# Kernel tuning notes

Hardware: AMD Instinct MI355X
Metric: run time of the kernel (lower is better)

The kernel has to match this reference:

```python
import jax, jax.numpy as jnp
import numpy as np

EPS = 1e-5

def _layernorm(x, gamma, beta):
    mu = jnp.mean(x, axis=-1, keepdims=True)
    var = jnp.mean(jnp.square(x - mu), axis=-1, keepdims=True)
    return (x - mu) * jax.lax.rsqrt(var + EPS) * gamma + beta

def setup_inputs() -> dict:
    key = jax.random.key(0)
    ks = jax.random.split(key, 8)
    B, T, H = 8, 4096, 512
    s = 1.0 / np.sqrt(H)  # torch LSTM init scale
    return {
        "x": jax.random.normal(ks[0], (B, T, H), jnp.float32),
        "W_ih": jax.random.uniform(ks[1], (4 * H, H), jnp.float32, -s, s),
        "W_hh": jax.random.uniform(ks[2], (4 * H, H), jnp.float32, -s, s),
        "b_ih": jax.random.uniform(ks[3], (4 * H,), jnp.float32, -s, s),
        "b_hh": jax.random.uniform(ks[4], (4 * H,), jnp.float32, -s, s),
        "gamma": jnp.ones((H,), jnp.float32),
        "beta": jnp.zeros((H,), jnp.float32),
        "W_lin": jax.random.uniform(ks[5], (H, H), jnp.float32, -s, s),
        "b_lin": jax.random.uniform(ks[6], (H,), jnp.float32, -s, s),
    }

def _lstm(res, W_ih, W_hh, b_ih, b_hh):
    # res: [B, T, H]; torch gate order: i, f, g, o
    B, T, H = res.shape
    # precompute input contributions for all timesteps: [T, B, 4H]
    x_proj = jnp.einsum('bth,gh->tbg', res, W_ih) + (b_ih + b_hh)

    def step(carry, xp):
        h, c = carry  # [B, H] each
        gates = xp + h @ W_hh.T  # [B, 4H]
        i, f, g, o = jnp.split(gates, 4, axis=-1)
        i = jax.nn.sigmoid(i)
        f = jax.nn.sigmoid(f)
        g = jnp.tanh(g)
        o = jax.nn.sigmoid(o)
        c = f * c + i * g
        h = o * jnp.tanh(c)
        return (h, c), h

    h0 = jnp.zeros((B, H), res.dtype)
    c0 = jnp.zeros((B, H), res.dtype)
    (hT, cT), hs = jax.lax.scan(step, (h0, c0), x_proj)
    out = jnp.transpose(hs, (1, 0, 2))  # [B, T, H]
    return out, (hT[None], cT[None])

def reference(x, W_ih, W_hh, b_ih, b_hh, gamma, beta, W_lin, b_lin):
    res = _layernorm(x, gamma, beta)
    out, out_state = _lstm(res, W_ih, W_hh, b_ih, b_hh)
    gate = jax.nn.silu(res @ W_lin.T + b_lin)
    out = out * gate + res
    return (out, out_state)
```

## Files before the change

### kernel.cpp

```cpp
#include <hip/hip_runtime.h>
#include <math.h>

#define NB 8
#define HID 512

typedef unsigned int uint4v __attribute__((ext_vector_type(4)));

__device__ __forceinline__ float sigf(float x) { return 1.0f / (1.0f + __expf(-x)); }
__device__ __forceinline__ float tanhf_(float x) {
    return 2.0f / (1.0f + __expf(-2.0f * x)) - 1.0f;
}

__global__ void init_ws_kernel(unsigned long long* h_bufs) {
    h_bufs[blockIdx.x * 256 + threadIdx.x] = 0ull;
}

__global__ void ln_kernel(const float* __restrict__ x, const float* __restrict__ gamma,
                          const float* __restrict__ beta, float* __restrict__ res,
                          int t0, int chsh) {
    int wid = threadIdx.x >> 6, lane = threadIdx.x & 63;
    int rl = blockIdx.x * 4 + wid;
    int b = rl >> chsh, i = rl & ((1 << chsh) - 1);
    const float* xr = x + (long long)(b * 4096 + t0 + i) * HID;
    float4 u0 = *(const float4*)(xr + lane * 4);
    float4 u1 = *(const float4*)(xr + 256 + lane * 4);
    float s = u0.x + u0.y + u0.z + u0.w + u1.x + u1.y + u1.z + u1.w;
#pragma unroll
    for (int m = 1; m < 64; m <<= 1) s += __shfl_xor(s, m, 64);
    float mu = s * (1.0f / 512.0f);
    float d[8] = {u0.x - mu, u0.y - mu, u0.z - mu, u0.w - mu,
                  u1.x - mu, u1.y - mu, u1.z - mu, u1.w - mu};
    float q = d[0]*d[0] + d[1]*d[1] + d[2]*d[2] + d[3]*d[3] +
              d[4]*d[4] + d[5]*d[5] + d[6]*d[6] + d[7]*d[7];
#pragma unroll
    for (int m = 1; m < 64; m <<= 1) q += __shfl_xor(q, m, 64);
    float rs = rsqrtf(q * (1.0f / 512.0f) + 1e-5f);
    float4 g0 = *(const float4*)(gamma + lane * 4);
    float4 g1 = *(const float4*)(gamma + 256 + lane * 4);
    float4 b0 = *(const float4*)(beta + lane * 4);
    float4 b1 = *(const float4*)(beta + 256 + lane * 4);
    float* rr = res + (long long)rl * HID;
    float4 o0, o1;
    o0.x = d[0] * rs * g0.x + b0.x; o0.y = d[1] * rs * g0.y + b0.y;
    o0.z = d[2] * rs * g0.z + b0.z; o0.w = d[3] * rs * g0.w + b0.w;
    o1.x = d[4] * rs * g1.x + b1.x; o1.y = d[5] * rs * g1.y + b1.y;
    o1.z = d[6] * rs * g1.z + b1.z; o1.w = d[7] * rs * g1.w + b1.w;
    *(float4*)(rr + lane * 4) = o0;
    *(float4*)(rr + 256 + lane * 4) = o1;
}

template <int MODE>
__launch_bounds__(256, 2)
__global__ void gemm_nt(const float* __restrict__ A, const float* __restrict__ B,
                        const float* __restrict__ bias1, const float* __restrict__ bias2,
                        float* __restrict__ C, int N) {
    __shared__ float As[16][132];
    __shared__ float Bs[16][132];
    int tid = threadIdx.x;
    int tx = tid & 15, ty = tid >> 4;
    int r0 = blockIdx.x * 128;
    int j0 = blockIdx.y * 128;
    int arow = tid >> 2, ac = (tid & 3) * 4;

    float acc[8][8] = {};

    for (int kt = 0; kt < 512; kt += 16) {
        float4 a0 = *(const float4*)(A + (long long)(r0 + arow) * 512 + kt + ac);
        float4 a1 = *(const float4*)(A + (long long)(r0 + arow + 64) * 512 + kt + ac);
        float4 b0 = *(const float4*)(B + (long long)(j0 + arow) * 512 + kt + ac);
        float4 b1 = *(const float4*)(B + (long long)(j0 + arow + 64) * 512 + kt + ac);
        __syncthreads();
        As[ac + 0][arow] = a0.x; As[ac + 1][arow] = a0.y;
        As[ac + 2][arow] = a0.z; As[ac + 3][arow] = a0.w;
        As[ac + 0][arow + 64] = a1.x; As[ac + 1][arow + 64] = a1.y;
        As[ac + 2][arow + 64] = a1.z; As[ac + 3][arow + 64] = a1.w;
        Bs[ac + 0][arow] = b0.x; Bs[ac + 1][arow] = b0.y;
        Bs[ac + 2][arow] = b0.z; Bs[ac + 3][arow] = b0.w;
        Bs[ac + 0][arow + 64] = b1.x; Bs[ac + 1][arow + 64] = b1.y;
        Bs[ac + 2][arow + 64] = b1.z; Bs[ac + 3][arow + 64] = b1.w;
        __syncthreads();
#pragma unroll
        for (int kk = 0; kk < 16; kk++) {
            float a[8], bb[8];
            *(float4*)(a)      = *(const float4*)&As[kk][ty * 8];
            *(float4*)(a + 4)  = *(const float4*)&As[kk][ty * 8 + 4];
            *(float4*)(bb)     = *(const float4*)&Bs[kk][tx * 8];
            *(float4*)(bb + 4) = *(const float4*)&Bs[kk][tx * 8 + 4];
#pragma unroll
            for (int i = 0; i < 8; i++)
#pragma unroll
                for (int j = 0; j < 8; j++) acc[i][j] += a[i] * bb[j];
        }
    }

    float bv[8];
#pragma unroll
    for (int jj = 0; jj < 8; jj++) {
        int j = j0 + tx * 8 + jj;
        bv[jj] = (MODE == 0) ? (bias1[j] + bias2[j]) : bias1[j];
    }
#pragma unroll
    for (int ii = 0; ii < 8; ii++) {
        long long r = r0 + ty * 8 + ii;
        float* crow = C + r * (long long)N + j0 + tx * 8;
        float v[8];
#pragma unroll
        for (int jj = 0; jj < 8; jj++) {
            float tv = acc[ii][jj] + bv[jj];
            if (MODE == 1) tv = tv * sigf(tv);
            v[jj] = tv;
        }
        float4 o0, o1;
        o0.x = v[0]; o0.y = v[1]; o0.z = v[2]; o0.w = v[3];
        o1.x = v[4]; o1.y = v[5]; o1.z = v[6]; o1.w = v[7];
        *(float4*)(crow) = o0;
        *(float4*)(crow + 4) = o1;
    }
}

__launch_bounds__(256, 1)
__global__ void scan_kernel(const float* __restrict__ W_hh,
                            const float* __restrict__ xp,
                            const float* __restrict__ resv,
                            const float* __restrict__ gatev,
                            float* __restrict__ out,
                            unsigned long long* __restrict__ h_fast,
                            unsigned long long* __restrict__ h_safe,
                            float* __restrict__ c_buf,
                            int t0, int chsh) {
    const int CH = 1 << chsh;
    int b = blockIdx.x & 7, w = blockIdx.x >> 3;
    int tid = threadIdx.x;
    int kg = tid & 15, rq = tid >> 4;
    int slot = w * 16 + rq;

    __shared__ __align__(16) float h_s[2][512];

    float wreg[4][32];
#pragma unroll
    for (int g = 0; g < 4; g++) {
        const float* wr = W_hh + (long long)((g << 9) + slot) * 512 + (kg << 5);
#pragma unroll
        for (int q = 0; q < 8; q++) {
            float4 u = *(const float4*)(wr + q * 4);
            wreg[g][q * 4 + 0] = u.x; wreg[g][q * 4 + 1] = u.y;
            wreg[g][q * 4 + 2] = u.z; wreg[g][q * 4 + 3] = u.w;
        }
    }

    float c_reg = 0.0f;
    if (t0 > 0 && kg == 0) c_reg = c_buf[(b << 9) + slot];

    int mode = 0;

    const int pr0 = 2 * tid;
    const int n_w  = tid >> 1;
    const int pg_w = (n_w & ~7) | ((n_w ^ (n_w >> 3)) & 7);
    const int fi_w = (pg_w << 2) | (pr0 & 3);

    for (int i = 0; i < CH; i++) {
        int t = t0 + i;
        int rl = (b << chsh) + i;

        float xpv0 = 0, xpv1 = 0, xpv2 = 0, xpv3 = 0, gv = 0, rv = 0;
        if (kg == 0) {
            const float* xr = xp + (long long)rl * 2048 + slot;
            xpv0 = xr[0]; xpv1 = xr[512]; xpv2 = xr[1024]; xpv3 = xr[1536];
            gv = gatev[rl * 512 + slot];
            rv = resv[rl * 512 + slot];
        }

        float acc0 = 0, acc1 = 0, acc2 = 0, acc3 = 0;
        if (t > 0) {
            const int par = (t - 1) & 1;
            const unsigned exp_tag = (unsigned)t;
            float h0 = 0.0f, h1 = 0.0f;
            bool got = false;

            if (mode == 0) {
                const unsigned long long* fb = h_fast + par * 4096 + (b << 9);
                uint4v p4;
                int tries = 0;
                while (true) {
                    asm volatile(
                        "global_load_dwordx4 %0, %1, off nt\n\t"
                        "s_waitcnt vmcnt(0)"
                        : "=v"(p4) : "v"(fb + pr0) : "memory");
                    if (p4[1] == exp_tag && p4[3] == exp_tag) {
                        h0 = __uint_as_float(p4[0]);
                        h1 = __uint_as_float(p4[2]);
                        got = true;
                        break;
                    }
                    if (++tries > 768) { mode = 1; break; }
                }
            }
            if (!got) {
                const unsigned long long* sb = h_safe + par * 4096 + (b << 9);
                unsigned long long v0 = 0, v1 = 0;
                if (mode == 1) {
                    bool g0 = false, g1 = false;
                    int tr = 0;
                    while (true) {
                        if (!g0) {
                            v0 = __hip_atomic_load(sb + pr0, __ATOMIC_RELAXED,
                                                   __HIP_MEMORY_SCOPE_AGENT);
                            g0 = ((unsigned)(v0 >> 32) == exp_tag);
                        }
                        if (!g1) {
                            v1 = __hip_atomic_load(sb + pr0 + 1, __ATOMIC_RELAXED,
                                                   __HIP_MEMORY_SCOPE_AGENT);
                            g1 = ((unsigned)(v1 >> 32) == exp_tag);
                        }
                        if (g0 && g1) break;
                        if (++tr > (1 << 15)) { mode = 2; break; }
                    }
                } else {
                    v0 = __hip_atomic_load(sb + pr0, __ATOMIC_RELAXED,
                                           __HIP_MEMORY_SCOPE_AGENT);
                    v1 = __hip_atomic_load(sb + pr0 + 1, __ATOMIC_RELAXED,
                                           __HIP_MEMORY_SCOPE_AGENT);
                }
                h0 = __uint_as_float((unsigned)v0);
                h1 = __uint_as_float((unsigned)v1);
            }

            int p = t & 1;
            *(float2*)&h_s[p][fi_w] = make_float2(h0, h1);
            __syncthreads();
            float hv[32];
#pragma unroll
            for (int q = 0; q < 8; q++) {
                int pg = (kg << 3) + (q ^ (kg & 7));
                float4 u = *(const float4*)&h_s[p][pg << 2];
                hv[q * 4 + 0] = u.x; hv[q * 4 + 1] = u.y;
                hv[q * 4 + 2] = u.z; hv[q * 4 + 3] = u.w;
            }
#pragma unroll
            for (int j = 0; j < 32; j++) {
                acc0 += hv[j] * wreg[0][j];
                acc1 += hv[j] * wreg[1][j];
                acc2 += hv[j] * wreg[2][j];
                acc3 += hv[j] * wreg[3][j];
            }
            acc0 += __shfl_xor(acc0, 1, 64); acc0 += __shfl_xor(acc0, 2, 64);
            acc0 += __shfl_xor(acc0, 4, 64); acc0 += __shfl_xor(acc0, 8, 64);
            acc1 += __shfl_xor(acc1, 1, 64); acc1 += __shfl_xor(acc1, 2, 64);
            acc1 += __shfl_xor(acc1, 4, 64); acc1 += __shfl_xor(acc1, 8, 64);
            acc2 += __shfl_xor(acc2, 1, 64); acc2 += __shfl_xor(acc2, 2, 64);
            acc2 += __shfl_xor(acc2, 4, 64); acc2 += __shfl_xor(acc2, 8, 64);
            acc3 += __shfl_xor(acc3, 1, 64); acc3 += __shfl_xor(acc3, 2, 64);
            acc3 += __shfl_xor(acc3, 4, 64); acc3 += __shfl_xor(acc3, 8, 64);
        }

        if (kg == 0) {
            float iv = sigf(acc0 + xpv0);
            float fv = sigf(acc1 + xpv1);
            float gt = tanhf_(acc2 + xpv2);
            float ov = sigf(acc3 + xpv3);
            c_reg = fv * c_reg + iv * gt;
            float h = ov * tanhf_(c_reg);
            unsigned long long pkt =
                ((unsigned long long)(unsigned)(t + 1) << 32) |
                (unsigned long long)__float_as_uint(h);
            __hip_atomic_store(h_safe + (t & 1) * 4096 + (b << 9) + slot, pkt,
                               __ATOMIC_RELAXED, __HIP_MEMORY_SCOPE_AGENT);
            unsigned long long* fp = h_fast + (t & 1) * 4096 + (b << 9) + slot;
            asm volatile("global_store_dwordx2 %0, %1, off sc0"
                         :: "v"(fp), "v"(pkt) : "memory");
            out[(long long)((b << 12) + t) * 512 + slot] = h * gv + rv;
            if (t == 4095) {
                out[16777216 + (b << 9) + slot] = h;
                out[16777216 + 4096 + (b << 9) + slot] = c_reg;
            }
            if (i == CH - 1) c_buf[(b << 9) + slot] = c_reg;
        }
    }
}

extern "C" void kernel_launch(void* const* d_in, const int* in_sizes, int n_in,
                              void* d_out, int out_size, void* d_ws, size_t ws_size,
                              hipStream_t stream) {
    const float* x     = (const float*)d_in[0];
    const float* W_ih  = (const float*)d_in[1];
    const float* W_hh  = (const float*)d_in[2];
    const float* b_ih  = (const float*)d_in[3];
    const float* b_hh  = (const float*)d_in[4];
    const float* gamma = (const float*)d_in[5];
    const float* beta  = (const float*)d_in[6];
    const float* W_lin = (const float*)d_in[7];
    const float* b_lin = (const float*)d_in[8];
    float* out = (float*)d_out;

    const size_t small_bytes = 16384ull * 8 + 4096ull * 4;
    int CH = 256;
    for (int cand = 4096; cand >= 256; cand >>= 1) {
        if ((size_t)98304 * cand + small_bytes <= ws_size) { CH = cand; break; }
    }
    int chsh = 31 - __builtin_clz(CH);

    float* ws      = (float*)d_ws;
    float* res_ch  = ws;
    float* gate_ch = res_ch + (size_t)8 * CH * 512;
    float* xp_ch   = gate_ch + (size_t)8 * CH * 512;
    unsigned long long* h_fast = (unsigned long long*)(xp_ch + (size_t)8 * CH * 2048);
    unsigned long long* h_safe = h_fast + 8192;
    float* c_buf   = (float*)(h_safe + 8192);

    init_ws_kernel<<<64, 256, 0, stream>>>(h_fast);

    int nchunks = 4096 / CH;
    for (int c = 0; c < nchunks; c++) {
        int t0 = c * CH;
        ln_kernel<<<8 * CH / 4, 256, 0, stream>>>(x, gamma, beta, res_ch, t0, chsh);
        gemm_nt<0><<<dim3(8 * CH / 128, 16), 256, 0, stream>>>(res_ch, W_ih, b_ih, b_hh,
                                                               xp_ch, 2048);
        gemm_nt<1><<<dim3(8 * CH / 128, 4), 256, 0, stream>>>(res_ch, W_lin, b_lin, b_lin,
                                                              gate_ch, 512);
        scan_kernel<<<256, 256, 0, stream>>>(W_hh, xp_ch, res_ch, gate_ch, out,
                                             h_fast, h_safe, c_buf, t0, chsh);
    }
}
```

Measured before the change: 7.330 ms.

## Prefetch xp/gate/res into double-buffered LDS and pipeline h polling loads

Result: faster. 6.702 ms (median of 2 runs) (-8.6%).

```diff
diff --git a/kernel.cpp b/kernel.cpp
--- a/kernel.cpp
+++ b/kernel.cpp
@@ -134,7 +134,11 @@
     int kg = tid & 15, rq = tid >> 4;
     int slot = w * 16 + rq;
 
-    __shared__ __align__(16) float h_s[2][512];
+    __shared__ __align__(16) float lds[13312];
+
+    const int ep_s = tid >> 2;
+    const int ep_g = tid & 3;
+    const int gr_s = tid & 63;
 
     float wreg[4][32];
 #pragma unroll
@@ -152,47 +156,69 @@
     if (t0 > 0 && kg == 0) c_reg = c_buf[(b << 9) + slot];
 
     int mode = 0;
-
     const int pr0 = 2 * tid;
     const int n_w  = tid >> 1;
     const int pg_w = (n_w & ~7) | ((n_w ^ (n_w >> 3)) & 7);
     const int fi_w = (pg_w << 2) | (pr0 & 3);
 
+    uint4v pa = {0, 0, 0, 0}, pb = {0, 0, 0, 0};
+    float4 pfx0 = {0,0,0,0}, pfx1 = {0,0,0,0}, pfx2 = {0,0,0,0}, pfx3 = {0,0,0,0};
+    float4 pfg0 = {0,0,0,0}, pfg1 = {0,0,0,0}, pfg2 = {0,0,0,0}, pfg3 = {0,0,0,0};
+
+    {
+        int row = (b << chsh) + ((ep_s < CH) ? ep_s : CH - 1);
+        const float* xr = xp + (long long)row * 2048 + (ep_g << 9) + (w << 4);
+        pfx0 = *(const float4*)(xr + 0);  pfx1 = *(const float4*)(xr + 4);
+        pfx2 = *(const float4*)(xr + 8);  pfx3 = *(const float4*)(xr + 12);
+        if (tid < 128) {
+            int row2 = (b << chsh) + gr_s;
+            const float* gr = (tid < 64 ? gatev : resv) + (long long)row2 * 512 + (w << 4);
+            pfg0 = *(const float4*)(gr + 0);  pfg1 = *(const float4*)(gr + 4);
+            pfg2 = *(const float4*)(gr + 8);  pfg3 = *(const float4*)(gr + 12);
+        }
+        asm volatile("s_waitcnt vmcnt(0)" ::: "memory");
+        float* xd = lds + 1024 + (ep_s << 6) + (ep_g << 4);
+        *(float4*)(xd + 0) = pfx0;  *(float4*)(xd + 4) = pfx1;
+        *(float4*)(xd + 8) = pfx2;  *(float4*)(xd + 12) = pfx3;
+        if (tid < 128) {
+            float* gd = lds + (tid < 64 ? 9216 : 11264) + (gr_s << 4);
+            *(float4*)(gd + 0) = pfg0;  *(float4*)(gd + 4) = pfg1;
+            *(float4*)(gd + 8) = pfg2;  *(float4*)(gd + 12) = pfg3;
+        }
+    }
+
     for (int i = 0; i < CH; i++) {
         int t = t0 + i;
-        int rl = (b << chsh) + i;
-
-        float xpv0 = 0, xpv1 = 0, xpv2 = 0, xpv3 = 0, gv = 0, rv = 0;
-        if (kg == 0) {
-            const float* xr = xp + (long long)rl * 2048 + slot;
-            xpv0 = xr[0]; xpv1 = xr[512]; xpv2 = xr[1024]; xpv3 = xr[1536];
-            gv = gatev[rl * 512 + slot];
-            rv = resv[rl * 512 + slot];
-        }
-
-        float acc0 = 0, acc1 = 0, acc2 = 0, acc3 = 0;
+        int es = i & 63;
+        int e = (i >> 6) & 1;
+        int p = t & 1;
+
+        float h0 = 0.0f, h1 = 0.0f;
         if (t > 0) {
             const int par = (t - 1) & 1;
             const unsigned exp_tag = (unsigned)t;
-            float h0 = 0.0f, h1 = 0.0f;
             bool got = false;
-
             if (mode == 0) {
-                const unsigned long long* fb = h_fast + par * 4096 + (b << 9);
-                uint4v p4;
+                const unsigned long long* fb = h_fast + par * 4096 + (b << 9) + pr0;
                 int tries = 0;
+                asm volatile("global_load_dwordx4 %0, %1, off nt"
+                             : "=v"(pa) : "v"(fb) : "memory");
                 while (true) {
-                    asm volatile(
-                        "global_load_dwordx4 %0, %1, off nt\n\t"
-                        "s_waitcnt vmcnt(0)"
-                        : "=v"(p4) : "v"(fb + pr0) : "memory");
-                    if (p4[1] == exp_tag && p4[3] == exp_tag) {
-                        h0 = __uint_as_float(p4[0]);
-                        h1 = __uint_as_float(p4[2]);
-                        got = true;
-                        break;
+                    asm volatile("global_load_dwordx4 %0, %1, off nt"
+                                 : "=v"(pb) : "v"(fb) : "memory");
+                    asm volatile("s_waitcnt vmcnt(1)" : "+v"(pa) :: "memory");
+                    if (pa[1] == exp_tag && pa[3] == exp_tag) {
+                        h0 = __uint_as_float(pa[0]); h1 = __uint_as_float(pa[2]);
+                        got = true; break;
                     }
-                    if (++tries > 768) { mode = 1; break; }
+                    asm volatile("global_load_dwordx4 %0, %1, off nt"
+                                 : "=v"(pa) : "v"(fb) : "memory");
+                    asm volatile("s_waitcnt vmcnt(1)" : "+v"(pb) :: "memory");
+                    if (pb[1] == exp_tag && pb[3] == exp_tag) {
+                        h0 = __uint_as_float(pb[0]); h1 = __uint_as_float(pb[2]);
+                        got = true; break;
+                    }
+                    if (++tries > 512) { mode = 1; break; }
                 }
             }
             if (!got) {
@@ -224,15 +250,46 @@
                 h0 = __uint_as_float((unsigned)v0);
                 h1 = __uint_as_float((unsigned)v1);
             }
-
-            int p = t & 1;
-            *(float2*)&h_s[p][fi_w] = make_float2(h0, h1);
-            __syncthreads();
+            *(float2*)&lds[(p << 9) + fi_w] = make_float2(h0, h1);
+        }
+
+        if (es == 0) {
+            int ib = i + 64;
+            int sx = ib + ep_s; if (sx > CH - 1) sx = CH - 1;
+            const float* xr = xp + (long long)((b << chsh) + sx) * 2048 + (ep_g << 9) + (w << 4);
+            pfx0 = *(const float4*)(xr + 0);  pfx1 = *(const float4*)(xr + 4);
+            pfx2 = *(const float4*)(xr + 8);  pfx3 = *(const float4*)(xr + 12);
+            if (tid < 128) {
+                int sy = ib + gr_s; if (sy > CH - 1) sy = CH - 1;
+                const float* gr = (tid < 64 ? gatev : resv) + (long long)((b << chsh) + sy) * 512 + (w << 4);
+                pfg0 = *(const float4*)(gr + 0);  pfg1 = *(const float4*)(gr + 4);
+                pfg2 = *(const float4*)(gr + 8);  pfg3 = *(const float4*)(gr + 12);
+            }
+        }
+        if (es == 1) {
+            asm volatile("s_waitcnt vmcnt(0)" ::: "memory");
+            int eo = e ^ 1;
+            float* xd = lds + 1024 + (eo << 12) + (ep_s << 6) + (ep_g << 4);
+            *(float4*)(xd + 0) = pfx0;  *(float4*)(xd + 4) = pfx1;
+            *(float4*)(xd + 8) = pfx2;  *(float4*)(xd + 12) = pfx3;
+            if (tid < 128) {
+                float* gd = lds + (tid < 64 ? 9216 : 11264) + (eo << 10) + (gr_s << 4);
+                *(float4*)(gd + 0) = pfg0;  *(float4*)(gd + 4) = pfg1;
+                *(float4*)(gd + 8) = pfg2;  *(float4*)(gd + 12) = pfg3;
+            }
+        }
+
+        asm volatile("s_waitcnt lgkmcnt(0)" ::: "memory");
+        __builtin_amdgcn_s_barrier();
+        asm volatile("" ::: "memory");
+
+        float acc0 = 0, acc1 = 0, acc2 = 0, acc3 = 0;
+        if (t > 0) {
             float hv[32];
 #pragma unroll
             for (int q = 0; q < 8; q++) {
                 int pg = (kg << 3) + (q ^ (kg & 7));
-                float4 u = *(const float4*)&h_s[p][pg << 2];
+                float4 u = *(const float4*)&lds[(p << 9) + (pg << 2)];
                 hv[q * 4 + 0] = u.x; hv[q * 4 + 1] = u.y;
                 hv[q * 4 + 2] = u.z; hv[q * 4 + 3] = u.w;
             }
@@ -254,6 +311,13 @@
         }
 
         if (kg == 0) {
+            const float* eb = lds + 1024 + (e << 12) + (es << 6);
+            float xpv0 = eb[rq];
+            float xpv1 = eb[16 + rq];
+            float xpv2 = eb[32 + rq];
+            float xpv3 = eb[48 + rq];
+            float gv = lds[9216 + (e << 10) + (es << 4) + rq];
+            float rv = lds[11264 + (e << 10) + (es << 4) + rq];
             float iv = sigf(acc0 + xpv0);
             float fv = sigf(acc1 + xpv1);
             float gt = tanhf_(acc2 + xpv2);
@@ -263,9 +327,9 @@
             unsigned long long pkt =
                 ((unsigned long long)(unsigned)(t + 1) << 32) |
                 (unsigned long long)__float_as_uint(h);
-            __hip_atomic_store(h_safe + (t & 1) * 4096 + (b << 9) + slot, pkt,
+            __hip_atomic_store(h_safe + p * 4096 + (b << 9) + slot, pkt,
                                __ATOMIC_RELAXED, __HIP_MEMORY_SCOPE_AGENT);
-            unsigned long long* fp = h_fast + (t & 1) * 4096 + (b << 9) + slot;
+            unsigned long long* fp = h_fast + p * 4096 + (b << 9) + slot;
             asm volatile("global_store_dwordx2 %0, %1, off sc0"
                          :: "v"(fp), "v"(pkt) : "memory");
             out[(long long)((b << 12) + t) * 512 + slot] = h * gv + rv;
@@ -276,6 +340,7 @@
             if (i == CH - 1) c_buf[(b << 9) + slot] = c_reg;
         }
     }
+    asm volatile("s_waitcnt vmcnt(0)" :: "v"(pa), "v"(pb) : "memory");
 }
 
 extern "C" void kernel_launch(void* const* d_in, const int* in_sizes, int n_in,
```
